# Optimization experiments

Measured on AMD Instinct MI355X. Metric: run time of the kernel, lower is better.

## Reference

```python
import jax, jax.numpy as jnp
import numpy as np

MAX_LEN = 4096

def causal_mask(seq_len, dtype=jnp.float32):
    # nn.Transformer.generate_square_subsequent_mask: 0 on/below diag, -inf above
    i = jnp.arange(seq_len)[:, None]
    j = jnp.arange(seq_len)[None, :]
    return jnp.where(j > i, -jnp.inf, 0.0).astype(dtype)

def setup_inputs() -> dict:
    key = jax.random.key(0)
    kq, kk, kv = jax.random.split(key, 3)
    B, H, S, D = 2, 8, 4096, 64
    q = jax.random.normal(kq, (B, H, S, D), dtype=jnp.float32)
    k = jax.random.normal(kk, (B, H, S, D), dtype=jnp.float32)
    v = jax.random.normal(kv, (B, H, S, D), dtype=jnp.float32)
    return {"q": q, "k": k, "v": v}

def reference(q, k, v):
    # q,k,v: [B,H,S,D]. Dropout is identity in eval mode.
    S = k.shape[2]
    D = k.shape[-1]
    scale = 1.0 / jnp.sqrt(jnp.asarray(D, dtype=q.dtype))
    scores = jnp.einsum('bhqd,bhkd->bhqk', q, k) * scale  # [B,H,S,S]
    scores = scores + causal_mask(S, scores.dtype)[None, None]
    probs = jax.nn.softmax(scores, axis=-1)
    return jnp.einsum('bhqk,bhkd->bhqd', probs, v)
```

## Files before the change

kernel.cpp:

```cpp
#include <hip/hip_runtime.h>


typedef __attribute__((ext_vector_type(8)))  short short8;
typedef __attribute__((ext_vector_type(16))) float floatx16;

#define S_LEN 4096
#define D_DIM 64
#define LOG2E 1.44269504088896340736f
#define M8L2  11.541560327111385f
#define PSTR  40

__device__ __forceinline__ unsigned short f2bf(float f) {
    union { float f; unsigned u; } x; x.f = f;
    unsigned u = x.u;
    u += 0x7fffu + ((u >> 16) & 1u);
    return (unsigned short)(u >> 16);
}

__device__ __forceinline__ float fast_exp2(float x) {
    float r;
    asm("v_exp_f32 %0, %1" : "=v"(r) : "v"(x));
    return r;
}

__device__ __forceinline__ void glds16(const void* g, void* l) {
    __builtin_amdgcn_global_load_lds(
        (const __attribute__((address_space(1))) unsigned int*)g,
        (__attribute__((address_space(3))) unsigned int*)l, 16, 0, 0);
}

__global__ __launch_bounds__(256) void prep_kv(
        const float* __restrict__ K, const float* __restrict__ V,
        unsigned short* __restrict__ img) {
    const int kt = blockIdx.x;
    const int bh = blockIdx.y;
    const int t  = threadIdx.x;
    const size_t inbase = (size_t)bh * (S_LEN * D_DIM) + (size_t)kt * (64 * D_DIM);
    unsigned short* out = img + ((size_t)bh * 64 + kt) * 8192;
    __shared__ __align__(16) unsigned short vt[64 * 72];
    #pragma unroll
    for (int i = 0; i < 2; ++i) {
        const int g   = i * 256 + t;
        const int key = g >> 3;
        const int d8  = (g & 7) * 8;
        const float* kp = K + inbase + key * 64 + d8;
        const float4 k0 = *(const float4*)kp;
        const float4 k1 = *(const float4*)(kp + 4);
        unsigned short ks8[8] = { f2bf(k0.x), f2bf(k0.y), f2bf(k0.z), f2bf(k0.w),
                                  f2bf(k1.x), f2bf(k1.y), f2bf(k1.z), f2bf(k1.w) };
        const int fk = (key >> 5) * 4 + (d8 >> 4);
        const int L  = ((d8 >> 3) & 1) * 32 + (key & 31);
        *(uint4*)(out + fk * 512 + L * 8) = *(const uint4*)ks8;
        const float* vp = V + inbase + key * 64 + d8;
        const float4 v0 = *(const float4*)vp;
        const float4 v1 = *(const float4*)(vp + 4);
        vt[(d8 + 0) * 72 + key] = f2bf(v0.x);
        vt[(d8 + 1) * 72 + key] = f2bf(v0.y);
        vt[(d8 + 2) * 72 + key] = f2bf(v0.z);
        vt[(d8 + 3) * 72 + key] = f2bf(v0.w);
        vt[(d8 + 4) * 72 + key] = f2bf(v1.x);
        vt[(d8 + 5) * 72 + key] = f2bf(v1.y);
        vt[(d8 + 6) * 72 + key] = f2bf(v1.z);
        vt[(d8 + 7) * 72 + key] = f2bf(v1.w);
    }
    __syncthreads();
    #pragma unroll
    for (int i = 0; i < 2; ++i) {
        const int o  = i * 256 + t;
        const int fv = o >> 6;
        const int L  = o & 63;
        const int d  = (fv >> 2) * 32 + (L & 31);
        const int kb = (fv & 3) * 16 + (L >> 5) * 8;
        *(uint4*)(out + 4096 + fv * 512 + L * 8) = *(const uint4*)&vt[d * 72 + kb];
    }
}

__global__ __launch_bounds__(256, 3) void fa_fwd(
        const float* __restrict__ Q, const unsigned short* __restrict__ img,
        float* __restrict__ O) {
    const int bh = blockIdx.x;
    const int qt = 63 - (int)blockIdx.y;
    const int tid  = threadIdx.x;
    const int wave = tid >> 6;
    const int lane = tid & 63;
    const int l31  = lane & 31;
    const int hl   = lane >> 5;
    const int wq   = wave >> 1;
    const int wk   = wave & 1;

    __shared__ __align__(16) unsigned short kv[2][8192];
    __shared__ __align__(16) unsigned short p_sh[4][32 * PSTR];

    const size_t base = (size_t)bh * (S_LEN * D_DIM);
    const int q0 = qt * 64;

    short8 qf[4];
    {
        const float* qp = Q + base + (size_t)(q0 + wq * 32 + l31) * D_DIM + hl * 8;
        #pragma unroll
        for (int ks = 0; ks < 4; ++ks) {
            const float4 f0 = *(const float4*)(qp + ks * 16);
            const float4 f1 = *(const float4*)(qp + ks * 16 + 4);
            short8 a;
            a[0] = (short)f2bf(f0.x * 0.125f); a[1] = (short)f2bf(f0.y * 0.125f);
            a[2] = (short)f2bf(f0.z * 0.125f); a[3] = (short)f2bf(f0.w * 0.125f);
            a[4] = (short)f2bf(f1.x * 0.125f); a[5] = (short)f2bf(f1.y * 0.125f);
            a[6] = (short)f2bf(f1.z * 0.125f); a[7] = (short)f2bf(f1.w * 0.125f);
            qf[ks] = a;
        }
    }

    floatx16 o_acc[2];
    #pragma unroll
    for (int n = 0; n < 2; ++n)
        #pragma unroll
        for (int r = 0; r < 16; ++r) o_acc[n][r] = 0.f;
    float lsum = 0.f;

    const unsigned short* tsrc = img + (size_t)bh * 64 * 8192;
    const int nkt = qt + 1;

    #define DMA_TILE(KT, BUF)                                                  \
        { const unsigned short* s_ = tsrc + (size_t)(KT) * 8192;               \
          _Pragma("unroll")                                                    \
          for (int i_ = 0; i_ < 4; ++i_) {                                     \
              const int f_ = wave * 4 + i_;                                    \
              glds16(s_ + f_ * 512 + lane * 8, (BUF) + f_ * 512 + lane * 8);   \
          } }

    DMA_TILE(0, kv[0])

    for (int kt = 0; kt < nkt; ++kt) {
        asm volatile("s_waitcnt vmcnt(0)" ::: "memory");
        __builtin_amdgcn_s_barrier();
        asm volatile("" ::: "memory");
        unsigned short* buf = kv[kt & 1];
        if (kt + 1 < nkt) DMA_TILE(kt + 1, kv[(kt + 1) & 1])

        const bool diag = (kt == nkt - 1);
        if (diag && wk > wq) continue;

        floatx16 s;
        #pragma unroll
        for (int r = 0; r < 16; ++r) s[r] = 0.f;
        #pragma unroll
        for (int ks = 0; ks < 4; ++ks) {
            const short8 ak = *(const short8*)&buf[(wk * 4 + ks) * 512 + lane * 8];
            s = __builtin_amdgcn_mfma_f32_32x32x16_bf16(ak, qf[ks], s, 0, 0, 0);
        }

        float p[16];
        #pragma unroll
        for (int r = 0; r < 16; ++r)
            p[r] = fast_exp2(fmaf(s[r], LOG2E, -M8L2));
        if (diag && wk == wq) {
            #pragma unroll
            for (int r = 0; r < 16; ++r) {
                const int row = (r & 3) + 8 * (r >> 2) + 4 * hl;
                p[r] = (row > l31) ? 0.f : p[r];
            }
        }
        #pragma unroll
        for (int r = 0; r < 16; ++r) lsum += p[r];
        unsigned short* pw = &p_sh[wave][l31 * PSTR];
        #pragma unroll
        for (int rg = 0; rg < 4; ++rg) {
            uint2 w;
            w.x = __builtin_amdgcn_perm(__float_as_uint(p[rg * 4 + 1]),
                                        __float_as_uint(p[rg * 4 + 0]), 0x07060302u);
            w.y = __builtin_amdgcn_perm(__float_as_uint(p[rg * 4 + 3]),
                                        __float_as_uint(p[rg * 4 + 2]), 0x07060302u);
            *(uint2*)&pw[rg * 8 + hl * 4] = w;
        }

        #pragma unroll
        for (int kk = 0; kk < 2; ++kk) {
            const short8 ap = *(const short8*)&p_sh[wave][l31 * PSTR + kk * 16 + hl * 8];
            #pragma unroll
            for (int nt = 0; nt < 2; ++nt) {
                const short8 bv = *(const short8*)&buf[4096 + (nt * 4 + 2 * wk + kk) * 512 + lane * 8];
                o_acc[nt] = __builtin_amdgcn_mfma_f32_32x32x16_bf16(ap, bv, o_acc[nt], 0, 0, 0);
            }
        }
    }
    #undef DMA_TILE

    lsum += __shfl_xor(lsum, 32);
    __syncthreads();
    float* ored = (float*)kv[0];
    float* lred = (float*)p_sh;
    if (lane < 32) lred[(wk * 2 + wq) * 32 + lane] = lsum;
    if (wk == 1) {
        #pragma unroll
        for (int nt = 0; nt < 2; ++nt)
            #pragma unroll
            for (int r = 0; r < 16; ++r) {
                const int q = (r & 3) + 8 * (r >> 2) + 4 * hl;
                ored[wq * 2048 + q * 64 + nt * 32 + l31] = o_acc[nt][r];
            }
    }
    __syncthreads();
    if (wk == 0) {
        #pragma unroll
        for (int r = 0; r < 16; ++r) {
            const int q = (r & 3) + 8 * (r >> 2) + 4 * hl;
            const float l = lred[wq * 32 + q] + lred[(2 + wq) * 32 + q];
            const float inv = 1.0f / l;
            #pragma unroll
            for (int nt = 0; nt < 2; ++nt) {
                const float v = (o_acc[nt][r] + ored[wq * 2048 + q * 64 + nt * 32 + l31]) * inv;
                O[base + (size_t)(q0 + wq * 32 + q) * D_DIM + nt * 32 + l31] = v;
            }
        }
    }
}

extern "C" void kernel_launch(void* const* d_in, const int* in_sizes, int n_in,
                              void* d_out, int out_size, void* d_ws, size_t ws_size,
                              hipStream_t stream) {
    const float* q = (const float*)d_in[0];
    const float* k = (const float*)d_in[1];
    const float* v = (const float*)d_in[2];
    float* o = (float*)d_out;
    (void)in_sizes; (void)n_in; (void)out_size; (void)ws_size;
    unsigned short* img = (unsigned short*)d_ws;
    hipLaunchKernelGGL(prep_kv, dim3(64, 16), dim3(256), 0, stream, k, v, img);
    hipLaunchKernelGGL(fa_fwd,  dim3(16, 64), dim3(256), 0, stream, q, img, o);
}
```

Baseline: 147.0 us.

## Double KV tile per DMA stage and remap blocks for XCD locality and balance

Each pipeline stage now loads two 64-key K/V tiles (128 keys) into LDS and processes them in an inner loop. This halves the number of barrier and wait iterations per block. The launch becomes a 1D grid whose block index is mapped so that each XCD handles two heads, improving L2 reuse of the KV image. Query tiles are interleaved heavy and light to balance the causal work. The LDS buffer doubles, and the occupancy hint drops from 3 to 2 blocks per CU, which may reduce latency hiding.

```diff
diff --git a/kernel.cpp b/kernel.cpp
--- a/kernel.cpp
+++ b/kernel.cpp
@@ -75,11 +75,22 @@
     }
 }
 
-__global__ __launch_bounds__(256, 3) void fa_fwd(
+__global__ __launch_bounds__(256, 2) void fa_fwd(
         const float* __restrict__ Q, const unsigned short* __restrict__ img,
         float* __restrict__ O) {
-    const int bh = blockIdx.x;
-    const int qt = 63 - (int)blockIdx.y;
+    const int x    = blockIdx.x;
+    const int xcd  = x & 7;
+    const int slot = x >> 3;
+    const int bh   = xcd * 2 + (slot & 1);
+    const int yy   = slot >> 1;
+    const int y0   = yy & 15;
+    int qt;
+    switch (yy >> 4) {
+        case 0:  qt = 63 - y0; break;
+        case 1:  qt = 47 - y0; break;
+        case 2:  qt = 16 + y0; break;
+        default: qt = y0;      break;
+    }
     const int tid  = threadIdx.x;
     const int wave = tid >> 6;
     const int lane = tid & 63;
@@ -88,7 +99,7 @@
     const int wq   = wave >> 1;
     const int wk   = wave & 1;
 
-    __shared__ __align__(16) unsigned short kv[2][8192];
+    __shared__ __align__(16) unsigned short kv[2][16384];
     __shared__ __align__(16) unsigned short p_sh[4][32 * PSTR];
 
     const size_t base = (size_t)bh * (S_LEN * D_DIM);
@@ -118,14 +129,14 @@
     float lsum = 0.f;
 
     const unsigned short* tsrc = img + (size_t)bh * 64 * 8192;
-    const int nkt = qt + 1;
+    const int nkt = (qt >> 1) + 1;
 
     #define DMA_TILE(KT, BUF)                                                  \
-        { const unsigned short* s_ = tsrc + (size_t)(KT) * 8192;               \
+        { const unsigned short* s_ = tsrc + (size_t)(KT) * 16384;              \
           _Pragma("unroll")                                                    \
-          for (int i_ = 0; i_ < 4; ++i_) {                                     \
-              const int f_ = wave * 4 + i_;                                    \
-              glds16(s_ + f_ * 512 + lane * 8, (BUF) + f_ * 512 + lane * 8);   \
+          for (int i_ = 0; i_ < 8; ++i_) {                                     \
+              const int c_ = wave * 8 + i_;                                    \
+              glds16(s_ + c_ * 512 + lane * 8, (BUF) + c_ * 512 + lane * 8);   \
           } }
 
     DMA_TILE(0, kv[0])
@@ -137,49 +148,55 @@
         unsigned short* buf = kv[kt & 1];
         if (kt + 1 < nkt) DMA_TILE(kt + 1, kv[(kt + 1) & 1])
 
-        const bool diag = (kt == nkt - 1);
-        if (diag && wk > wq) continue;
-
-        floatx16 s;
-        #pragma unroll
-        for (int r = 0; r < 16; ++r) s[r] = 0.f;
-        #pragma unroll
-        for (int ks = 0; ks < 4; ++ks) {
-            const short8 ak = *(const short8*)&buf[(wk * 4 + ks) * 512 + lane * 8];
-            s = __builtin_amdgcn_mfma_f32_32x32x16_bf16(ak, qf[ks], s, 0, 0, 0);
-        }
-
-        float p[16];
-        #pragma unroll
-        for (int r = 0; r < 16; ++r)
-            p[r] = fast_exp2(fmaf(s[r], LOG2E, -M8L2));
-        if (diag && wk == wq) {
-            #pragma unroll
-            for (int r = 0; r < 16; ++r) {
-                const int row = (r & 3) + 8 * (r >> 2) + 4 * hl;
-                p[r] = (row > l31) ? 0.f : p[r];
-            }
-        }
-        #pragma unroll
-        for (int r = 0; r < 16; ++r) lsum += p[r];
-        unsigned short* pw = &p_sh[wave][l31 * PSTR];
-        #pragma unroll
-        for (int rg = 0; rg < 4; ++rg) {
-            uint2 w;
-            w.x = __builtin_amdgcn_perm(__float_as_uint(p[rg * 4 + 1]),
-                                        __float_as_uint(p[rg * 4 + 0]), 0x07060302u);
-            w.y = __builtin_amdgcn_perm(__float_as_uint(p[rg * 4 + 3]),
-                                        __float_as_uint(p[rg * 4 + 2]), 0x07060302u);
-            *(uint2*)&pw[rg * 8 + hl * 4] = w;
-        }
-
-        #pragma unroll
-        for (int kk = 0; kk < 2; ++kk) {
-            const short8 ap = *(const short8*)&p_sh[wave][l31 * PSTR + kk * 16 + hl * 8];
-            #pragma unroll
-            for (int nt = 0; nt < 2; ++nt) {
-                const short8 bv = *(const short8*)&buf[4096 + (nt * 4 + 2 * wk + kk) * 512 + lane * 8];
-                o_acc[nt] = __builtin_amdgcn_mfma_f32_32x32x16_bf16(ap, bv, o_acc[nt], 0, 0, 0);
+        #pragma unroll
+        for (int h = 0; h < 2; ++h) {
+            const int t64 = kt * 2 + h;
+            if (t64 > qt) continue;
+            const bool diag = (t64 == qt);
+            if (diag && wk > wq) continue;
+            const unsigned short* hbuf = buf + h * 8192;
+
+            floatx16 s;
+            #pragma unroll
+            for (int r = 0; r < 16; ++r) s[r] = 0.f;
+            #pragma unroll
+            for (int ks = 0; ks < 4; ++ks) {
+                const short8 ak = *(const short8*)&hbuf[(wk * 4 + ks) * 512 + lane * 8];
+                s = __builtin_amdgcn_mfma_f32_32x32x16_bf16(ak, qf[ks], s, 0, 0, 0);
+            }
+
+            float p[16];
+            #pragma unroll
+            for (int r = 0; r < 16; ++r)
+                p[r] = fast_exp2(fmaf(s[r], LOG2E, -M8L2));
+            if (diag && wk == wq) {
+                #pragma unroll
+                for (int r = 0; r < 16; ++r) {
+                    const int row = (r & 3) + 8 * (r >> 2) + 4 * hl;
+                    p[r] = (row > l31) ? 0.f : p[r];
+                }
+            }
+            #pragma unroll
+            for (int r = 0; r < 16; ++r) lsum += p[r];
+            unsigned short* pw = &p_sh[wave][l31 * PSTR];
+            #pragma unroll
+            for (int rg = 0; rg < 4; ++rg) {
+                uint2 w;
+                w.x = __builtin_amdgcn_perm(__float_as_uint(p[rg * 4 + 1]),
+                                            __float_as_uint(p[rg * 4 + 0]), 0x07060302u);
+                w.y = __builtin_amdgcn_perm(__float_as_uint(p[rg * 4 + 3]),
+                                            __float_as_uint(p[rg * 4 + 2]), 0x07060302u);
+                *(uint2*)&pw[rg * 8 + hl * 4] = w;
+            }
+
+            #pragma unroll
+            for (int kk = 0; kk < 2; ++kk) {
+                const short8 ap = *(const short8*)&p_sh[wave][l31 * PSTR + kk * 16 + hl * 8];
+                #pragma unroll
+                for (int nt = 0; nt < 2; ++nt) {
+                    const short8 bv = *(const short8*)&hbuf[4096 + (nt * 4 + 2 * wk + kk) * 512 + lane * 8];
+                    o_acc[nt] = __builtin_amdgcn_mfma_f32_32x32x16_bf16(ap, bv, o_acc[nt], 0, 0, 0);
+                }
             }
         }
     }
@@ -225,5 +242,5 @@
     (void)in_sizes; (void)n_in; (void)out_size; (void)ws_size;
     unsigned short* img = (unsigned short*)d_ws;
     hipLaunchKernelGGL(prep_kv, dim3(64, 16), dim3(256), 0, stream, k, v, img);
-    hipLaunchKernelGGL(fa_fwd,  dim3(16, 64), dim3(256), 0, stream, q, img, o);
-}
+    hipLaunchKernelGGL(fa_fwd,  dim3(1024), dim3(256), 0, stream, q, img, o);
+}
```

After: 155.6 us. +5.8%, slower.
